# Optimization experiments

Measured on AMD Instinct MI355X. Metric: run time of the kernel, lower is better.

Reference implementation:

```python
import jax, jax.numpy as jnp
import numpy as np

B, L, E, H = 2, 4096, 1024, 16
D = E // H          # head_dim = 64
CHUNK = 256         # matches the torch module's chunk_size


def setup_inputs() -> dict:
    key = jax.random.key(0)
    k1, k2, k3 = jax.random.split(key, 3)
    x = jax.random.normal(k1, (B, L, E), dtype=jnp.float32)
    # torch Linear weight layout: (out_features, in_features); y = x @ W.T
    W_qkv = jax.random.normal(k2, (3 * E, E), dtype=jnp.float32) * 0.02
    W_out = jax.random.normal(k3, (E, E), dtype=jnp.float32) * 0.02
    return {"x": x, "W_qkv": W_qkv, "W_out": W_out}


def _linear_attention(x, W_qkv, W_out):
    Bz, Lz, Ez = x.shape
    scale = D ** (-0.5)
    qkv = x @ W_qkv.T                                # [B, L, 3E]
    qkv = qkv.reshape(Bz, Lz, 3, H, D).transpose(2, 0, 3, 1, 4)  # [3, B, H, L, D]
    q, k, v = qkv[0], qkv[1], qkv[2]
    # feature map: elu(x) + 1, query also scaled by head_dim^-0.5
    q = (jax.nn.elu(q) + 1.0) * scale
    k = jax.nn.elu(k) + 1.0

    nc = Lz // CHUNK  # seq_len chosen divisible by CHUNK
    def to_chunks(t):  # [B,H,L,D] -> [nc, B, H, CHUNK, D]
        return t.reshape(Bz, H, nc, CHUNK, D).transpose(2, 0, 1, 3, 4)
    qc, kc, vc = to_chunks(q), to_chunks(k), to_chunks(v)

    causal = jnp.tril(jnp.ones((CHUNK, CHUNK), dtype=x.dtype))

    def step(carry, inp):
        S, Z = carry                     # S: [B,H,D,D], Z: [B,H,D]
        qi, ki, vi = inp                 # each [B,H,CHUNK,D]
        # intra-chunk causal contribution (same math as cumsum of k v^T outer products)
        attn = jnp.einsum('bhld,bhmd->bhlm', qi, ki) * causal
        num = jnp.einsum('bhlm,bhme->bhle', attn, vi) + jnp.einsum('bhld,bhde->bhle', qi, S)
        den = attn.sum(-1) + jnp.einsum('bhld,bhd->bhl', qi, Z)
        S = S + jnp.einsum('bhmd,bhme->bhde', ki, vi)
        Z = Z + ki.sum(axis=2)
        return (S, Z), (num, den)

    S0 = jnp.zeros((Bz, H, D, D), dtype=x.dtype)
    Z0 = jnp.zeros((Bz, H, D), dtype=x.dtype)
    _, (num, den) = jax.lax.scan(step, (S0, Z0), (qc, kc, vc))
    # [nc,B,H,CHUNK,D] -> [B,H,L,D]
    num = num.transpose(1, 2, 0, 3, 4).reshape(Bz, H, Lz, D)
    den = den.transpose(1, 2, 0, 3).reshape(Bz, H, Lz)
    den = jnp.maximum(den, 1e-6)
    out = num / den[..., None]
    out = out.transpose(0, 2, 1, 3).reshape(Bz, Lz, Ez)
    return out @ W_out.T


def reference(x, W_qkv, W_out):
    return _linear_attention(x, W_qkv, W_out)
```

## Files before the change

### kernel.cpp

```cpp
#include <hip/hip_runtime.h>
#include <hip/hip_bf16.h>
#include <math.h>

#define B_ 2
#define L_ 4096
#define E_ 1024
#define H_ 16
#define D_ 64
#define CK_ 64
#define NC_ 64

typedef __bf16 bf16x8 __attribute__((ext_vector_type(8)));
typedef __bf16 bf16x4 __attribute__((ext_vector_type(4)));
typedef float  f32x4  __attribute__((ext_vector_type(4)));

__device__ __forceinline__ float fmap1(float x) { return x > 0.f ? x + 1.f : expf(x); }
__device__ __forceinline__ float ldf(const __hip_bfloat16* p) { return __bfloat162float(*p); }
__device__ __forceinline__ __bf16 f2b(float f) {
    __hip_bfloat16 h = __float2bfloat16(f); return *reinterpret_cast<__bf16*>(&h);
}
__device__ __forceinline__ unsigned short f2u(float f) {
    __hip_bfloat16 h = __float2bfloat16(f); return *reinterpret_cast<unsigned short*>(&h);
}

union U8 { bf16x8 v; __bf16 e[8]; bf16x4 half2[2]; };

__device__ __forceinline__ void async16(const __bf16* g, __bf16* lds) {
    __builtin_amdgcn_global_load_lds(
        (const __attribute__((address_space(1))) void*)g,
        (__attribute__((address_space(3))) void*)lds, 16, 0, 0);
}

__global__ __launch_bounds__(256) void cast_f32_bf16(const float* __restrict__ in,
                                                     __hip_bfloat16* __restrict__ out, int n) {
    int i = (blockIdx.x * 256 + threadIdx.x) << 2;
    if (i < n) {
        float4 v = *(const float4*)(in + i);
        ushort4 o = {f2u(v.x), f2u(v.y), f2u(v.z), f2u(v.w)};
        *(ushort4*)(out + i) = o;
    }
}

template<int EPI>
__global__ __launch_bounds__(256) void gemm_mfma(const __bf16* __restrict__ A,
                                                 const __bf16* __restrict__ Bw,
                                                 void* __restrict__ Cv,
                                                 __hip_bfloat16* __restrict__ VT,
                                                 int M, int N, int K) {
    __shared__ alignas(16) __bf16 As[128 * 32];
    __shared__ alignas(16) __bf16 Bs[128 * 32];
    const int tid = threadIdx.x;
    const int wave = tid >> 6, lane = tid & 63;
    const int wm = wave >> 1, wn = wave & 1;
    const int lq = lane >> 4, lr = lane & 15;
    const int m0 = blockIdx.y * 128, n0 = blockIdx.x * 128;

    f32x4 acc[4][4];
#pragma unroll
    for (int i = 0; i < 4; ++i)
#pragma unroll
        for (int j = 0; j < 4; ++j) acc[i][j] = (f32x4){0.f, 0.f, 0.f, 0.f};

    const int stg_r = lane >> 2, stg_c = (lane & 3) << 3;
    const __bf16* Ag0 = A + (size_t)(m0 + (wave << 4) + stg_r) * K + stg_c;
    const __bf16* Ag1 = A + (size_t)(m0 + 64 + (wave << 4) + stg_r) * K + stg_c;
    const __bf16* Bg0 = Bw + (size_t)(n0 + (wave << 4) + stg_r) * K + stg_c;
    const __bf16* Bg1 = Bw + (size_t)(n0 + 64 + (wave << 4) + stg_r) * K + stg_c;
    __bf16* Al0 = As + (wave << 9);
    __bf16* Al1 = As + ((wave + 4) << 9);
    __bf16* Bl0 = Bs + (wave << 9);
    __bf16* Bl1 = Bs + ((wave + 4) << 9);

    for (int kt = 0; kt < K; kt += 32) {
        __syncthreads();
        async16(Ag0 + kt, Al0);
        async16(Ag1 + kt, Al1);
        async16(Bg0 + kt, Bl0);
        async16(Bg1 + kt, Bl1);
        __syncthreads();
        bf16x8 af[4], bfr[4];
#pragma unroll
        for (int t = 0; t < 4; ++t) {
            af[t]  = *(const bf16x8*)&As[((wm << 6) + (t << 4) + lr) * 32 + (lq << 3)];
            bfr[t] = *(const bf16x8*)&Bs[((wn << 6) + (t << 4) + lr) * 32 + (lq << 3)];
        }
#pragma unroll
        for (int mt = 0; mt < 4; ++mt)
#pragma unroll
            for (int nt = 0; nt < 4; ++nt)
                acc[mt][nt] = __builtin_amdgcn_mfma_f32_16x16x32_bf16(
                    af[mt], bfr[nt], acc[mt][nt], 0, 0, 0);
    }

#pragma unroll
    for (int mt = 0; mt < 4; ++mt) {
#pragma unroll
        for (int nt = 0; nt < 4; ++nt) {
            int m = m0 + (wm << 6) + (mt << 4) + (lq << 2);
            int n = n0 + (wn << 6) + (nt << 4) + lr;
            if (EPI == 1) {
                int w = n >> 10, hh = (n >> 6) & 15, dd = n & 63;
                float vv[4];
#pragma unroll
                for (int r = 0; r < 4; ++r) {
                    float v = acc[mt][nt][r];
                    if (w == 0)      v = fmap1(v) * 0.125f;
                    else if (w == 1) v = fmap1(v);
                    vv[r] = v;
                    ((__hip_bfloat16*)Cv)[(size_t)(m + r) * N + n] = __float2bfloat16(v);
                }
                if (w == 2) {
                    int b = m >> 12, l = m & 4095;
                    ushort4 u = {f2u(vv[0]), f2u(vv[1]), f2u(vv[2]), f2u(vv[3])};
                    *(ushort4*)&VT[((size_t)((b * 16 + hh) * 64 + dd) << 12) + l] = u;
                }
            } else {
#pragma unroll
                for (int r = 0; r < 4; ++r)
                    ((float*)Cv)[(size_t)(m + r) * N + n] = acc[mt][nt][r];
            }
        }
    }
}

__global__ __launch_bounds__(256) void chunk_state64(const __hip_bfloat16* __restrict__ qv,
                                                     float* __restrict__ S,
                                                     float* __restrict__ Z) {
    __shared__ float kl[64], vl[64];
    const int c = blockIdx.x, bh = blockIdx.y, b = bh >> 4, h = bh & 15;
    const int tid = threadIdx.x;
    float acc[16];
#pragma unroll
    for (int t = 0; t < 16; ++t) acc[t] = 0.f;
    float zacc = 0.f;
    for (int l = 0; l < CK_; ++l) {
        const __hip_bfloat16* base = qv + (size_t)(b * L_ + c * CK_ + l) * 3072 + h * 64;
        if (tid < 64) kl[tid] = ldf(&base[1024 + tid]);
        else if (tid < 128) vl[tid - 64] = ldf(&base[2048 + (tid - 64)]);
        __syncthreads();
        if (tid < 64) zacc += kl[tid];
#pragma unroll
        for (int t = 0; t < 16; ++t) {
            int pair = tid + t * 256;
            acc[t] += vl[pair >> 6] * kl[pair & 63];
        }
        __syncthreads();
    }
    float* Sp = S + ((size_t)(c * 32 + bh) << 12);
#pragma unroll
    for (int t = 0; t < 16; ++t) Sp[tid + t * 256] = acc[t];
    if (tid < 64) Z[((c * 32 + bh) << 6) + tid] = zacc;
}

__global__ __launch_bounds__(256) void prefix64(float* __restrict__ S,
                                                float* __restrict__ Z) {
    const int bh = blockIdx.y;
    const int idx = blockIdx.x * 256 + threadIdx.x;
    float run = 0.f;
    for (int c = 0; c < NC_; ++c) {
        size_t off = ((size_t)(c * 32 + bh) << 12) + idx;
        float cur = S[off];
        S[off] = run;
        run += cur;
    }
    if (blockIdx.x == 0 && threadIdx.x < 64) {
        float zr = 0.f;
        for (int c = 0; c < NC_; ++c) {
            int zoff = ((c * 32 + bh) << 6) + threadIdx.x;
            float cz = Z[zoff];
            Z[zoff] = zr;
            zr += cz;
        }
    }
}

__global__ __launch_bounds__(256) void attn_out_mfma(const __hip_bfloat16* __restrict__ qvh,
                                                     const float* __restrict__ S,
                                                     const float* __restrict__ Z,
                                                     const __hip_bfloat16* __restrict__ VTh,
                                                     __hip_bfloat16* __restrict__ attn) {
    __shared__ __bf16 Pbuf[4 * 64 * 68];
    const int tid = threadIdx.x, wave = tid >> 6, lane = tid & 63;
    const int quad = lane >> 4, lr = lane & 15;
    const int bh = blockIdx.y, b = bh >> 4, h = bh & 15;
    const int c = blockIdx.x * 4 + wave;
    const size_t t0 = (size_t)b * L_ + c * CK_;
    const __bf16* qb = (const __bf16*)qvh;
    const __bf16* VT = (const __bf16*)VTh;
    __bf16* P = Pbuf + wave * (64 * 68);

    bf16x8 qf[4][2];
#pragma unroll
    for (int ls = 0; ls < 4; ++ls)
#pragma unroll
        for (int kk = 0; kk < 2; ++kk)
            qf[ls][kk] = *(const bf16x8*)&qb[(t0 + ls * 16 + lr) * 3072 + h * 64 + kk * 32 + quad * 8];

    f32x4 num[4][4], den[4];
#pragma unroll
    for (int i = 0; i < 4; ++i) {
        den[i] = (f32x4){0.f, 0.f, 0.f, 0.f};
#pragma unroll
        for (int j = 0; j < 4; ++j) num[i][j] = (f32x4){0.f, 0.f, 0.f, 0.f};
    }

    const float* Zp = Z + ((size_t)(c * 32 + bh) << 6);
    U8 zf[2];
#pragma unroll
    for (int kk = 0; kk < 2; ++kk)
#pragma unroll
        for (int j = 0; j < 8; ++j) zf[kk].e[j] = f2b(Zp[kk * 32 + quad * 8 + j]);
#pragma unroll
    for (int ls = 0; ls < 4; ++ls)
#pragma unroll
        for (int kk = 0; kk < 2; ++kk)
            den[ls] = __builtin_amdgcn_mfma_f32_16x16x32_bf16(qf[ls][kk], zf[kk].v, den[ls], 0, 0, 0);

    const float* Sp = S + ((size_t)(c * 32 + bh) << 12);
#pragma unroll
    for (int es = 0; es < 4; ++es) {
        U8 sf[2];
#pragma unroll
        for (int kk = 0; kk < 2; ++kk) {
            const float* p = &Sp[(es * 16 + lr) * 64 + kk * 32 + quad * 8];
#pragma unroll
            for (int j = 0; j < 8; ++j) sf[kk].e[j] = f2b(p[j]);
        }
#pragma unroll
        for (int ls = 0; ls < 4; ++ls)
#pragma unroll
            for (int kk = 0; kk < 2; ++kk)
                num[ls][es] = __builtin_amdgcn_mfma_f32_16x16x32_bf16(
                    qf[ls][kk], sf[kk].v, num[ls][es], 0, 0, 0);
    }

    bf16x8 kf[4][2];
#pragma unroll
    for (int ms = 0; ms < 4; ++ms)
#pragma unroll
        for (int kk = 0; kk < 2; ++kk)
            kf[ms][kk] = *(const bf16x8*)&qb[(t0 + ms * 16 + lr) * 3072 + 1024 + h * 64 + kk * 32 + quad * 8];

#pragma unroll
    for (int ls = 0; ls < 4; ++ls) {
#pragma unroll
        for (int ms = 0; ms < 4; ++ms) {
            int off = (ls * 16 + lr) * 68 + ms * 16 + quad * 4;
            if (ms <= ls) {
                f32x4 pt = (f32x4){0.f, 0.f, 0.f, 0.f};
                pt = __builtin_amdgcn_mfma_f32_16x16x32_bf16(kf[ms][0], qf[ls][0], pt, 0, 0, 0);
                pt = __builtin_amdgcn_mfma_f32_16x16x32_bf16(kf[ms][1], qf[ls][1], pt, 0, 0, 0);
                ushort4 u;
                if (ms == ls) {
                    u.x = (quad * 4 + 0 > lr) ? 0 : f2u(pt[0]);
                    u.y = (quad * 4 + 1 > lr) ? 0 : f2u(pt[1]);
                    u.z = (quad * 4 + 2 > lr) ? 0 : f2u(pt[2]);
                    u.w = (quad * 4 + 3 > lr) ? 0 : f2u(pt[3]);
                } else {
                    u = (ushort4){f2u(pt[0]), f2u(pt[1]), f2u(pt[2]), f2u(pt[3])};
                }
                *(ushort4*)&P[off] = u;
            } else {
                *(ushort4*)&P[off] = (ushort4){0, 0, 0, 0};
            }
        }
    }

    U8 of;
#pragma unroll
    for (int j = 0; j < 8; ++j) of.e[j] = f2b(1.0f);

#pragma unroll
    for (int kk = 0; kk < 2; ++kk) {
        U8 pf[4];
#pragma unroll
        for (int ls = 0; ls < 4; ++ls) {
            pf[ls].half2[0] = *(const bf16x4*)&P[(ls * 16 + lr) * 68 + kk * 32 + quad * 8];
            pf[ls].half2[1] = *(const bf16x4*)&P[(ls * 16 + lr) * 68 + kk * 32 + quad * 8 + 4];
        }
        bf16x8 vf[4];
#pragma unroll
        for (int es = 0; es < 4; ++es)
            vf[es] = *(const bf16x8*)&VT[((size_t)((b * 16 + h) * 64 + es * 16 + lr) << 12)
                                         + c * CK_ + kk * 32 + quad * 8];
#pragma unroll
        for (int ls = 0; ls < 4; ++ls) {
            den[ls] = __builtin_amdgcn_mfma_f32_16x16x32_bf16(pf[ls].v, of.v, den[ls], 0, 0, 0);
#pragma unroll
            for (int es = 0; es < 4; ++es)
                num[ls][es] = __builtin_amdgcn_mfma_f32_16x16x32_bf16(
                    pf[ls].v, vf[es], num[ls][es], 0, 0, 0);
        }
    }

#pragma unroll
    for (int ls = 0; ls < 4; ++ls) {
#pragma unroll
        for (int r = 0; r < 4; ++r) {
            float inv = 1.f / fmaxf(den[ls][r], 1e-6f);
            size_t row = (t0 + ls * 16 + quad * 4 + r) * 1024 + h * 64;
#pragma unroll
            for (int es = 0; es < 4; ++es)
                attn[row + es * 16 + lr] = __float2bfloat16(num[ls][es][r] * inv);
        }
    }
}

extern "C" void kernel_launch(void* const* d_in, const int* in_sizes, int n_in,
                              void* d_out, int out_size, void* d_ws, size_t ws_size,
                              hipStream_t stream) {
    (void)ws_size; (void)out_size;
    const float *x = nullptr, *Wqkv = nullptr, *Wout = nullptr;
    for (int i = 0; i < n_in; ++i) {
        if (in_sizes[i] == 8388608)      x    = (const float*)d_in[i];
        else if (in_sizes[i] == 3145728) Wqkv = (const float*)d_in[i];
        else if (in_sizes[i] == 1048576) Wout = (const float*)d_in[i];
    }

    __hip_bfloat16* ws16  = (__hip_bfloat16*)d_ws;
    __hip_bfloat16* xb    = ws16;
    __hip_bfloat16* attn  = ws16;
    __hip_bfloat16* Wqkvb = ws16 + 8388608;
    __hip_bfloat16* Woutb = Wqkvb + 3145728;
    __hip_bfloat16* qv    = Woutb + 1048576;
    __hip_bfloat16* VT    = qv + 25165824;
    float* S = (float*)(VT + 8388608);
    float* Z = S + 8388608;

    cast_f32_bf16<<<8388608 / 1024, 256, 0, stream>>>(x, xb, 8388608);
    cast_f32_bf16<<<3145728 / 1024, 256, 0, stream>>>(Wqkv, Wqkvb, 3145728);
    cast_f32_bf16<<<1048576 / 1024, 256, 0, stream>>>(Wout, Woutb, 1048576);

    gemm_mfma<1><<<dim3(3072 / 128, 8192 / 128), 256, 0, stream>>>(
        (const __bf16*)xb, (const __bf16*)Wqkvb, qv, VT, B_ * L_, 3 * E_, E_);
    chunk_state64<<<dim3(NC_, B_ * H_), 256, 0, stream>>>(qv, S, Z);
    prefix64<<<dim3(16, B_ * H_), 256, 0, stream>>>(S, Z);
    attn_out_mfma<<<dim3(16, B_ * H_), 256, 0, stream>>>(qv, S, Z, VT, attn);
    gemm_mfma<0><<<dim3(1024 / 128, 8192 / 128), 256, 0, stream>>>(
        (const __bf16*)attn, (const __bf16*)Woutb, d_out, nullptr, B_ * L_, E_, E_);
}
```

Baseline: 285.8 us.

## Compute per-chunk KV state with MFMA from transposed K/V and store state in bf16

```diff
diff --git a/kernel.cpp b/kernel.cpp
--- a/kernel.cpp
+++ b/kernel.cpp
@@ -15,7 +15,9 @@
 typedef float  f32x4  __attribute__((ext_vector_type(4)));
 
 __device__ __forceinline__ float fmap1(float x) { return x > 0.f ? x + 1.f : expf(x); }
-__device__ __forceinline__ float ldf(const __hip_bfloat16* p) { return __bfloat162float(*p); }
+__device__ __forceinline__ float b2f(__bf16 v) {
+    __hip_bfloat16 h = *reinterpret_cast<__hip_bfloat16*>(&v); return __bfloat162float(h);
+}
 __device__ __forceinline__ __bf16 f2b(float f) {
     __hip_bfloat16 h = __float2bfloat16(f); return *reinterpret_cast<__bf16*>(&h);
 }
@@ -45,6 +47,7 @@
 __global__ __launch_bounds__(256) void gemm_mfma(const __bf16* __restrict__ A,
                                                  const __bf16* __restrict__ Bw,
                                                  void* __restrict__ Cv,
+                                                 __hip_bfloat16* __restrict__ KT,
                                                  __hip_bfloat16* __restrict__ VT,
                                                  int M, int N, int K) {
     __shared__ alignas(16) __bf16 As[128 * 32];
@@ -109,10 +112,11 @@
                     vv[r] = v;
                     ((__hip_bfloat16*)Cv)[(size_t)(m + r) * N + n] = __float2bfloat16(v);
                 }
-                if (w == 2) {
+                if (w >= 1) {
                     int b = m >> 12, l = m & 4095;
+                    __hip_bfloat16* T = (w == 1) ? KT : VT;
                     ushort4 u = {f2u(vv[0]), f2u(vv[1]), f2u(vv[2]), f2u(vv[3])};
-                    *(ushort4*)&VT[((size_t)((b * 16 + hh) * 64 + dd) << 12) + l] = u;
+                    *(ushort4*)&T[((size_t)((b * 16 + hh) * 64 + dd) << 12) + l] = u;
                 }
             } else {
 #pragma unroll
@@ -123,60 +127,83 @@
     }
 }
 
-__global__ __launch_bounds__(256) void chunk_state64(const __hip_bfloat16* __restrict__ qv,
-                                                     float* __restrict__ S,
-                                                     float* __restrict__ Z) {
-    __shared__ float kl[64], vl[64];
-    const int c = blockIdx.x, bh = blockIdx.y, b = bh >> 4, h = bh & 15;
-    const int tid = threadIdx.x;
-    float acc[16];
-#pragma unroll
-    for (int t = 0; t < 16; ++t) acc[t] = 0.f;
-    float zacc = 0.f;
-    for (int l = 0; l < CK_; ++l) {
-        const __hip_bfloat16* base = qv + (size_t)(b * L_ + c * CK_ + l) * 3072 + h * 64;
-        if (tid < 64) kl[tid] = ldf(&base[1024 + tid]);
-        else if (tid < 128) vl[tid - 64] = ldf(&base[2048 + (tid - 64)]);
-        __syncthreads();
-        if (tid < 64) zacc += kl[tid];
-#pragma unroll
-        for (int t = 0; t < 16; ++t) {
-            int pair = tid + t * 256;
-            acc[t] += vl[pair >> 6] * kl[pair & 63];
-        }
-        __syncthreads();
-    }
-    float* Sp = S + ((size_t)(c * 32 + bh) << 12);
-#pragma unroll
-    for (int t = 0; t < 16; ++t) Sp[tid + t * 256] = acc[t];
-    if (tid < 64) Z[((c * 32 + bh) << 6) + tid] = zacc;
-}
-
-__global__ __launch_bounds__(256) void prefix64(float* __restrict__ S,
-                                                float* __restrict__ Z) {
+__global__ __launch_bounds__(256) void chunk_state_mfma(const __hip_bfloat16* __restrict__ KTh,
+                                                        const __hip_bfloat16* __restrict__ VTh,
+                                                        __hip_bfloat16* __restrict__ Sb,
+                                                        __hip_bfloat16* __restrict__ Zb) {
+    const int tid = threadIdx.x, wave = tid >> 6, lane = tid & 63;
+    const int quad = lane >> 4, lr = lane & 15;
+    const int bh = blockIdx.y;
+    const int c = blockIdx.x * 4 + wave;
+    const __bf16* KT = (const __bf16*)KTh;
+    const __bf16* VT = (const __bf16*)VTh;
+
+    bf16x8 vt[4][2], kt[4][2];
+#pragma unroll
+    for (int t = 0; t < 4; ++t)
+#pragma unroll
+        for (int kk = 0; kk < 2; ++kk) {
+            size_t rowoff = ((size_t)(bh * 64 + t * 16 + lr) << 12) + c * CK_ + kk * 32 + quad * 8;
+            vt[t][kk] = *(const bf16x8*)&VT[rowoff];
+            kt[t][kk] = *(const bf16x8*)&KT[rowoff];
+        }
+
+    U8 of;
+#pragma unroll
+    for (int j = 0; j < 8; ++j) of.e[j] = f2b(1.0f);
+
+    __hip_bfloat16* Sp = Sb + ((size_t)(c * 32 + bh) << 12);
+#pragma unroll
+    for (int es = 0; es < 4; ++es) {
+#pragma unroll
+        for (int dt = 0; dt < 4; ++dt) {
+            f32x4 acc = (f32x4){0.f, 0.f, 0.f, 0.f};
+            acc = __builtin_amdgcn_mfma_f32_16x16x32_bf16(vt[es][0], kt[dt][0], acc, 0, 0, 0);
+            acc = __builtin_amdgcn_mfma_f32_16x16x32_bf16(vt[es][1], kt[dt][1], acc, 0, 0, 0);
+#pragma unroll
+            for (int r = 0; r < 4; ++r)
+                Sp[(es * 16 + quad * 4 + r) * 64 + dt * 16 + lr] =
+                    __float2bfloat16(acc[r]);
+        }
+    }
+#pragma unroll
+    for (int dt = 0; dt < 4; ++dt) {
+        f32x4 z = (f32x4){0.f, 0.f, 0.f, 0.f};
+        z = __builtin_amdgcn_mfma_f32_16x16x32_bf16(kt[dt][0], of.v, z, 0, 0, 0);
+        z = __builtin_amdgcn_mfma_f32_16x16x32_bf16(kt[dt][1], of.v, z, 0, 0, 0);
+        if (lr == 0) {
+#pragma unroll
+            for (int r = 0; r < 4; ++r)
+                Zb[((c * 32 + bh) << 6) + dt * 16 + quad * 4 + r] = __float2bfloat16(z[r]);
+        }
+    }
+}
+
+__global__ __launch_bounds__(256) void prefix64(__hip_bfloat16* __restrict__ Sb,
+                                                __hip_bfloat16* __restrict__ Zb) {
     const int bh = blockIdx.y;
     const int idx = blockIdx.x * 256 + threadIdx.x;
     float run = 0.f;
     for (int c = 0; c < NC_; ++c) {
         size_t off = ((size_t)(c * 32 + bh) << 12) + idx;
-        float cur = S[off];
-        S[off] = run;
+        float cur = __bfloat162float(Sb[off]);
+        Sb[off] = __float2bfloat16(run);
         run += cur;
     }
     if (blockIdx.x == 0 && threadIdx.x < 64) {
         float zr = 0.f;
         for (int c = 0; c < NC_; ++c) {
             int zoff = ((c * 32 + bh) << 6) + threadIdx.x;
-            float cz = Z[zoff];
-            Z[zoff] = zr;
+            float cz = __bfloat162float(Zb[zoff]);
+            Zb[zoff] = __float2bfloat16(zr);
             zr += cz;
         }
     }
 }
 
 __global__ __launch_bounds__(256) void attn_out_mfma(const __hip_bfloat16* __restrict__ qvh,
-                                                     const float* __restrict__ S,
-                                                     const float* __restrict__ Z,
+                                                     const __hip_bfloat16* __restrict__ Sbh,
+                                                     const __hip_bfloat16* __restrict__ Zbh,
                                                      const __hip_bfloat16* __restrict__ VTh,
                                                      __hip_bfloat16* __restrict__ attn) {
     __shared__ __bf16 Pbuf[4 * 64 * 68];
@@ -186,6 +213,8 @@
     const int c = blockIdx.x * 4 + wave;
     const size_t t0 = (size_t)b * L_ + c * CK_;
     const __bf16* qb = (const __bf16*)qvh;
+    const __bf16* Sb = (const __bf16*)Sbh;
+    const __bf16* Zb = (const __bf16*)Zbh;
     const __bf16* VT = (const __bf16*)VTh;
     __bf16* P = Pbuf + wave * (64 * 68);
 
@@ -204,34 +233,29 @@
         for (int j = 0; j < 4; ++j) num[i][j] = (f32x4){0.f, 0.f, 0.f, 0.f};
     }
 
-    const float* Zp = Z + ((size_t)(c * 32 + bh) << 6);
-    U8 zf[2];
+    bf16x8 zf[2];
 #pragma unroll
     for (int kk = 0; kk < 2; ++kk)
-#pragma unroll
-        for (int j = 0; j < 8; ++j) zf[kk].e[j] = f2b(Zp[kk * 32 + quad * 8 + j]);
+        zf[kk] = *(const bf16x8*)&Zb[((size_t)(c * 32 + bh) << 6) + kk * 32 + quad * 8];
 #pragma unroll
     for (int ls = 0; ls < 4; ++ls)
 #pragma unroll
         for (int kk = 0; kk < 2; ++kk)
-            den[ls] = __builtin_amdgcn_mfma_f32_16x16x32_bf16(qf[ls][kk], zf[kk].v, den[ls], 0, 0, 0);
-
-    const float* Sp = S + ((size_t)(c * 32 + bh) << 12);
+            den[ls] = __builtin_amdgcn_mfma_f32_16x16x32_bf16(qf[ls][kk], zf[kk], den[ls], 0, 0, 0);
+
 #pragma unroll
     for (int es = 0; es < 4; ++es) {
-        U8 sf[2];
-#pragma unroll
-        for (int kk = 0; kk < 2; ++kk) {
-            const float* p = &Sp[(es * 16 + lr) * 64 + kk * 32 + quad * 8];
-#pragma unroll
-            for (int j = 0; j < 8; ++j) sf[kk].e[j] = f2b(p[j]);
-        }
+        bf16x8 sf[2];
+#pragma unroll
+        for (int kk = 0; kk < 2; ++kk)
+            sf[kk] = *(const bf16x8*)&Sb[((size_t)(c * 32 + bh) << 12)
+                                         + (es * 16 + lr) * 64 + kk * 32 + quad * 8];
 #pragma unroll
         for (int ls = 0; ls < 4; ++ls)
 #pragma unroll
             for (int kk = 0; kk < 2; ++kk)
                 num[ls][es] = __builtin_amdgcn_mfma_f32_16x16x32_bf16(
-                    qf[ls][kk], sf[kk].v, num[ls][es], 0, 0, 0);
+                    qf[ls][kk], sf[kk], num[ls][es], 0, 0, 0);
     }
 
     bf16x8 kf[4][2];
@@ -324,18 +348,19 @@
     __hip_bfloat16* Woutb = Wqkvb + 3145728;
     __hip_bfloat16* qv    = Woutb + 1048576;
     __hip_bfloat16* VT    = qv + 25165824;
-    float* S = (float*)(VT + 8388608);
-    float* Z = S + 8388608;
+    __hip_bfloat16* KT    = VT + 8388608;
+    __hip_bfloat16* Sb    = KT + 8388608;
+    __hip_bfloat16* Zb    = Sb + 8388608;
 
     cast_f32_bf16<<<8388608 / 1024, 256, 0, stream>>>(x, xb, 8388608);
     cast_f32_bf16<<<3145728 / 1024, 256, 0, stream>>>(Wqkv, Wqkvb, 3145728);
     cast_f32_bf16<<<1048576 / 1024, 256, 0, stream>>>(Wout, Woutb, 1048576);
 
     gemm_mfma<1><<<dim3(3072 / 128, 8192 / 128), 256, 0, stream>>>(
-        (const __bf16*)xb, (const __bf16*)Wqkvb, qv, VT, B_ * L_, 3 * E_, E_);
-    chunk_state64<<<dim3(NC_, B_ * H_), 256, 0, stream>>>(qv, S, Z);
-    prefix64<<<dim3(16, B_ * H_), 256, 0, stream>>>(S, Z);
-    attn_out_mfma<<<dim3(16, B_ * H_), 256, 0, stream>>>(qv, S, Z, VT, attn);
+        (const __bf16*)xb, (const __bf16*)Wqkvb, qv, KT, VT, B_ * L_, 3 * E_, E_);
+    chunk_state_mfma<<<dim3(16, B_ * H_), 256, 0, stream>>>(KT, VT, Sb, Zb);
+    prefix64<<<dim3(16, B_ * H_), 256, 0, stream>>>(Sb, Zb);
+    attn_out_mfma<<<dim3(16, B_ * H_), 256, 0, stream>>>(qv, Sb, Zb, VT, attn);
     gemm_mfma<0><<<dim3(1024 / 128, 8192 / 128), 256, 0, stream>>>(
-        (const __bf16*)attn, (const __bf16*)Woutb, d_out, nullptr, B_ * L_, E_, E_);
-}
+        (const __bf16*)attn, (const __bf16*)Woutb, d_out, nullptr, nullptr, B_ * L_, E_, E_);
+}
```

New measurement: 251.0 us. 1.14x faster.
